# Performance work log

Hardware: AMD Instinct MI355X
Metric: run time of the kernel (lower is better)

The kernel has to match this reference:

```python
import jax, jax.numpy as jnp
import numpy as np

N = 50000        # nodes
E_RAND = 800000  # random edges (plus N self-loops)
NFEAT = 128
NHID = 64
NCLASS = 64
NHEADS = 8
ALPHA = 0.2      # leaky_relu negative slope


def setup_inputs() -> dict:
    key = jax.random.key(0)
    ks = jax.random.split(key, 7)
    x = jax.random.normal(ks[0], (N, NFEAT), jnp.float32)
    src = jax.random.randint(ks[1], (E_RAND,), 0, N, dtype=jnp.int32)
    dst = jax.random.randint(ks[2], (E_RAND,), 0, N, dtype=jnp.int32)
    loops = jnp.arange(N, dtype=jnp.int32)  # self-loops so every row has mass
    edge_index = jnp.stack([jnp.concatenate([src, loops]),
                            jnp.concatenate([dst, loops])], axis=0)  # [2, E]
    W1 = jax.random.normal(ks[3], (NHEADS, NFEAT, NHID), jnp.float32) / np.sqrt(NFEAT).astype(np.float32)
    a1 = jax.random.normal(ks[4], (NHEADS, 2 * NHID), jnp.float32) * 0.1
    W2 = jax.random.normal(ks[5], (NHEADS, NHID * NHEADS, NCLASS // NHEADS), jnp.float32) / np.sqrt(NHID * NHEADS).astype(np.float32)
    a2 = jax.random.normal(ks[6], (NHEADS, 2 * (NCLASS // NHEADS)), jnp.float32) * 0.1
    return {"x": x, "edge_index": edge_index, "W1": W1, "a1": a1, "W2": W2, "a2": a2}


def _sp_gat_head(x, src, dst, W, a):
    # SpGraphAttentionLayer (concat=True), eval mode (no dropout).
    h = x @ W                          # [N, F]
    F = h.shape[1]
    # a . [h_src || h_dst] decomposed into per-node terms (avoids [E, 2F] concat)
    s_src = h @ a[:F]                  # [N]
    s_dst = h @ a[F:]                  # [N]
    z = s_src[src] + s_dst[dst]        # [E] edge scores
    e = jnp.exp(-jax.nn.leaky_relu(z, ALPHA))  # [E] unnormalized attention
    n = h.shape[0]
    rowsum = jax.ops.segment_sum(e, src, num_segments=n)                      # [N]
    num = jax.ops.segment_sum(e[:, None] * h[dst], src, num_segments=n)       # [N, F]
    return jax.nn.elu(num / rowsum[:, None])


def reference(x, edge_index, W1, a1, W2, a2):
    src, dst = edge_index[0], edge_index[1]
    # layer 1: heads concat along feature dim -> [N, NHID*NHEADS]
    h1 = jnp.concatenate([_sp_gat_head(x, src, dst, W1[i], a1[i]) for i in range(NHEADS)], axis=1)
    # layer 2: heads concat -> [N, NCLASS]
    h2 = jnp.concatenate([_sp_gat_head(h1, src, dst, W2[i], a2[i]) for i in range(NHEADS)], axis=1)
    return h2
```

## Files before the change

kernel.cpp:

```cpp
#include <hip/hip_runtime.h>
#include <math.h>

typedef unsigned int u32;
typedef unsigned short u16;
typedef __attribute__((ext_vector_type(8))) short bf16x8;
typedef __attribute__((ext_vector_type(4))) float f32x4;
typedef __attribute__((ext_vector_type(2))) float f32x2;

static constexpr int TNFEAT  = 128;
static constexpr int TNHEADS = 8;
static constexpr int C1      = 512;
static constexpr int C2      = 64;

__device__ inline float bf2f(u16 u) {
  union { u32 i; float f; } c; c.i = ((u32)u) << 16; return c.f;
}
__device__ inline float bitsf(u32 u) {
  union { u32 i; float f; } c; c.i = u; return c.f;
}
__device__ inline u16 f2bf(float f) {
  union { float f; u32 i; } c; c.f = f;
  u32 r = c.i + 0x7FFF + ((c.i >> 16) & 1);
  return (u16)(r >> 16);
}
__device__ inline u32 cvt_pk_bf16(float lo, float hi) {
  u32 r;
  asm volatile("v_cvt_pk_bf16_f32 %0, %1, %2" : "=v"(r) : "v"(lo), "v"(hi));
  return r;
}
__device__ inline uint4 ld16(const u16* base, u32 byteoff) {
  return *reinterpret_cast<const uint4*>(reinterpret_cast<const char*>(base) + byteoff);
}
__device__ inline f32x2 up2(u32 q) {
  f32x2 p;
  p.x = bitsf(q << 16);
  p.y = bitsf(q & 0xffff0000u);
  return p;
}
__device__ inline float elu_fast(float v) {
  return v > 0.f ? v : (__expf(v) - 1.f);
}
__device__ inline int rdl_i(int v, int l) { return __builtin_amdgcn_readlane(v, l); }
__device__ inline float rdl_f(float v, int l) {
  union { float f; int i; } c; c.f = v;
  union { int i; float f; } d; d.i = __builtin_amdgcn_readlane(c.i, l);
  return d.f;
}

__global__ void k_zero(int* __restrict__ p, int n) {
  int i = blockIdx.x * blockDim.x + threadIdx.x;
  if (i < n) p[i] = 0;
}

__global__ void k_hist(const int* __restrict__ src, int* __restrict__ deg, int E) {
  int i = blockIdx.x * blockDim.x + threadIdx.x;
  if (i < E) atomicAdd(&deg[src[i]], 1);
}

__global__ __launch_bounds__(1024) void k_bscan1(const int* __restrict__ deg,
                                                 int* __restrict__ loc,
                                                 int* __restrict__ bsum, int n) {
  __shared__ int sdata[1024];
  int t = threadIdx.x;
  int i = blockIdx.x * 1024 + t;
  int v = (i < n) ? deg[i] : 0;
  sdata[t] = v;
  __syncthreads();
  for (int ofs = 1; ofs < 1024; ofs <<= 1) {
    int tv = (t >= ofs) ? sdata[t - ofs] : 0;
    __syncthreads();
    sdata[t] += tv;
    __syncthreads();
  }
  if (i < n) loc[i] = sdata[t];
  if (t == 1023) bsum[blockIdx.x] = sdata[1023];
}

__global__ void k_bscan2(int* __restrict__ bsum, int nb) {
  int t = threadIdx.x;
  int v = (t < nb) ? bsum[t] : 0;
  #pragma unroll
  for (int ofs = 1; ofs < 64; ofs <<= 1) {
    int u = __shfl_up(v, ofs);
    if (t >= ofs) v += u;
  }
  if (t < nb) bsum[t] = v;
}

__global__ __launch_bounds__(1024) void k_offs(const int* __restrict__ loc,
                                               const int* __restrict__ bsum,
                                               const int* __restrict__ deg,
                                               int* __restrict__ offs,
                                               int* __restrict__ cur, int n) {
  int b = blockIdx.x;
  int i = b * 1024 + threadIdx.x;
  int base = (b > 0) ? bsum[b - 1] : 0;
  if (i < n) {
    int v = base + loc[i];
    offs[i + 1] = v;
    cur[i] = v - deg[i];
  }
  if (i == 0) offs[0] = 0;
}

__global__ void k_fill(const int* __restrict__ src, const int* __restrict__ dst,
                       int* __restrict__ cur, int* __restrict__ adj, int E) {
  int i = blockIdx.x * blockDim.x + threadIdx.x;
  if (i < E) {
    int p = atomicAdd(&cur[src[i]], 1);
    adj[p] = dst[i];
  }
}

__global__ void k_packAll(const float* __restrict__ W1, const float* __restrict__ W2,
                          const float* __restrict__ a1,
                          u16* __restrict__ w1hi, u16* __restrict__ w1lo,
                          u16* __restrict__ w2hi, u16* __restrict__ w2lo,
                          u16* __restrict__ vhi, u16* __restrict__ vlo) {
  int b = blockIdx.x;
  if (b < 256) {
    int idx = b * 256 + threadIdx.x;
    int j = idx & 7, lane = (idx >> 3) & 63, ks = (idx >> 9) & 3, cg = idx >> 11;
    int col = cg * 16 + (lane & 15);
    int k = ks * 32 + (lane >> 4) * 8 + j;
    float f = W1[((size_t)(col >> 6) * 128 + k) * 64 + (col & 63)];
    u16 h = f2bf(f);
    w1hi[idx] = h;
    w1lo[idx] = f2bf(f - bf2f(h));
  } else if (b < 384) {
    int idx = (b - 256) * 256 + threadIdx.x;
    int j = idx & 7, lane = (idx >> 3) & 63, ks = (idx >> 9) & 15, cg = idx >> 13;
    int col = cg * 16 + (lane & 15);
    int k = ks * 32 + (lane >> 4) * 8 + j;
    float f = W2[((size_t)(col >> 3) * 512 + k) * 8 + (col & 7)];
    u16 h = f2bf(f);
    w2hi[idx] = h;
    w2lo[idx] = f2bf(f - bf2f(h));
  } else {
    int idx = (b - 384) * 256 + threadIdx.x;
    int j = idx & 7, lane = (idx >> 3) & 63, ks = idx >> 9;
    int k = ks * 32 + (lane >> 4) * 8 + j;
    int c = lane & 15;
    int h = c >> 1, s = c & 1;
    const float* wrow = W1 + ((size_t)h * 128 + k) * 64;
    const float* av = a1 + h * 128 + s * 64;
    float dot = 0.f;
    #pragma unroll 8
    for (int f = 0; f < 64; f++) dot = fmaf(wrow[f], av[f], dot);
    u16 hb = f2bf(dot);
    vhi[idx] = hb;
    vlo[idx] = f2bf(dot - bf2f(hb));
  }
}

__global__ __launch_bounds__(256) void k_xprep(const float* __restrict__ x,
        const u16* __restrict__ vhi, const u16* __restrict__ vlo,
        u16* __restrict__ xb, float* __restrict__ ss, float* __restrict__ sd, int N) {
  int w = threadIdx.x >> 6, lane = threadIdx.x & 63;
  int lr = lane & 15, lk = lane >> 4;
  int row0 = blockIdx.x * 64 + w * 16;
  f32x4 acc = {0.f, 0.f, 0.f, 0.f};
  for (int ks = 0; ks < 4; ++ks) {
    int row = row0 + lr;
    int rc = row < N ? row : 0;
    const float* ap = x + (size_t)rc * 128 + ks * 32 + lk * 8;
    float4 f0 = *reinterpret_cast<const float4*>(ap);
    float4 f1 = *reinterpret_cast<const float4*>(ap + 4);
    float fa[8] = {f0.x, f0.y, f0.z, f0.w, f1.x, f1.y, f1.z, f1.w};
    union { u32 u[4]; bf16x8 v; uint4 q; } ch, cl;
    #pragma unroll
    for (int p = 0; p < 4; ++p) {
      float e0 = fa[2 * p], e1 = fa[2 * p + 1];
      u32 h = cvt_pk_bf16(e0, e1);
      ch.u[p] = h;
      cl.u[p] = cvt_pk_bf16(e0 - bitsf(h << 16), e1 - bitsf(h & 0xffff0000u));
    }
    if (row < N)
      *reinterpret_cast<uint4*>(&xb[(size_t)row * 128 + ks * 32 + lk * 8]) = ch.q;
    size_t bidx = ((size_t)ks * 64 + lane) * 8;
    bf16x8 Bh = *reinterpret_cast<const bf16x8*>(&vhi[bidx]);
    bf16x8 Bl = *reinterpret_cast<const bf16x8*>(&vlo[bidx]);
    acc = __builtin_amdgcn_mfma_f32_16x16x32_bf16(ch.v, Bh, acc, 0, 0, 0);
    acc = __builtin_amdgcn_mfma_f32_16x16x32_bf16(cl.v, Bh, acc, 0, 0, 0);
    acc = __builtin_amdgcn_mfma_f32_16x16x32_bf16(ch.v, Bl, acc, 0, 0, 0);
  }
  int h = lr >> 1, s = lr & 1;
  float* dstp = (s == 0) ? ss : sd;
  #pragma unroll
  for (int r = 0; r < 4; ++r) {
    int row = row0 + lk * 4 + r;
    if (row < N) dstp[row * 8 + h] = acc[r];
  }
}

__global__ __launch_bounds__(256) void k_agg1x(const u16* __restrict__ xb,
        const float* __restrict__ ss, const float* __restrict__ sd,
        const int* __restrict__ offs, const int* __restrict__ adj,
        u16* __restrict__ g, int n) {
  int node = (blockIdx.x * 256 + threadIdx.x) >> 6;
  int lane = threadIdx.x & 63;
  if (node >= n) return;
  int head = lane >> 3, li = lane & 7;
  int beg = offs[node], end = offs[node + 1];
  float sS = ss[node * 8 + head];
  const char* xbb = reinterpret_cast<const char*>(xb);
  f32x2 acc2[8] = {};
  float rsum = 0.f;
  int e = beg;
  for (; e + 8 <= end; e += 8) {
    int dl = adj[e + li];
    float z = sS + sd[(u32)dl * 8u + head];
    float w = __expf(-(z > 0.f ? z : 0.2f * z));
    rsum += w;
    u32 qv[8];
    #pragma unroll
    for (int i = 0; i < 8; i++) {
      u32 di = (u32)rdl_i(dl, i);
      qv[i] = *reinterpret_cast<const u32*>(xbb + di * 256u + lane * 4u);
    }
    #pragma unroll
    for (int i = 0; i < 8; i++) {
      f32x2 xv = up2(qv[i]);
      #pragma unroll
      for (int h2 = 0; h2 < 8; h2++) {
        float wi = rdl_f(w, h2 * 8 + i);
        acc2[h2] += (f32x2){wi, wi} * xv;
      }
    }
  }
  if (e < end) {
    int m = end - e;
    int lic = li < m ? li : m - 1;
    int dl = adj[e + lic];
    float z = sS + sd[(u32)dl * 8u + head];
    float w = __expf(-(z > 0.f ? z : 0.2f * z));
    if (li >= m) w = 0.f;
    rsum += w;
    u32 qv[8];
    #pragma unroll
    for (int i = 0; i < 8; i++) {
      if (i < m) {
        u32 di = (u32)rdl_i(dl, i);
        qv[i] = *reinterpret_cast<const u32*>(xbb + di * 256u + lane * 4u);
      }
    }
    #pragma unroll
    for (int i = 0; i < 8; i++) {
      if (i < m) {
        f32x2 xv = up2(qv[i]);
        #pragma unroll
        for (int h2 = 0; h2 < 8; h2++) {
          float wi = rdl_f(w, h2 * 8 + i);
          acc2[h2] += (f32x2){wi, wi} * xv;
        }
      }
    }
  }
  rsum += __shfl_xor(rsum, 1);
  rsum += __shfl_xor(rsum, 2);
  rsum += __shfl_xor(rsum, 4);
  float inv = 1.f / rsum;
  u32* gu = reinterpret_cast<u32*>(g);
  #pragma unroll
  for (int h2 = 0; h2 < 8; h2++) {
    float ih = rdl_f(inv, h2 * 8);
    gu[((size_t)node * 8 + h2) * 64 + lane] = cvt_pk_bf16(acc2[h2].x * ih, acc2[h2].y * ih);
  }
}

__global__ __launch_bounds__(256) void k_gemm12(const u16* __restrict__ g,
        const u16* __restrict__ w1h, const u16* __restrict__ w1l,
        const u16* __restrict__ w2h, const u16* __restrict__ w2l,
        const float* __restrict__ a2,
        u16* __restrict__ h2p, float* __restrict__ ss2, float* __restrict__ sd2,
        int N) {
  __shared__ u16 h1t[32][516];
  int w = threadIdx.x >> 6, lane = threadIdx.x & 63;
  int lr = lane & 15, lk = lane >> 4;
  int row0 = blockIdx.x * 32;
  for (int hh = 0; hh < 2; ++hh) {
    int head = 2 * w + hh;
    f32x4 acc[2][4] = {};
    for (int ks = 0; ks < 4; ++ks) {
      bf16x8 Ah[2];
      #pragma unroll
      for (int rf = 0; rf < 2; ++rf) {
        int row = row0 + rf * 16 + lr;
        int rc = row < N ? row : 0;
        Ah[rf] = *reinterpret_cast<const bf16x8*>(
            &g[((size_t)rc * 8 + head) * 128 + ks * 32 + lk * 8]);
      }
      #pragma unroll
      for (int cf = 0; cf < 4; ++cf) {
        size_t bidx = ((size_t)((head * 4 + cf) * 4 + ks) * 64 + lane) * 8;
        bf16x8 Bh = *reinterpret_cast<const bf16x8*>(&w1h[bidx]);
        bf16x8 Bl = *reinterpret_cast<const bf16x8*>(&w1l[bidx]);
        #pragma unroll
        for (int rf = 0; rf < 2; ++rf) {
          acc[rf][cf] = __builtin_amdgcn_mfma_f32_16x16x32_bf16(Ah[rf], Bh, acc[rf][cf], 0, 0, 0);
          acc[rf][cf] = __builtin_amdgcn_mfma_f32_16x16x32_bf16(Ah[rf], Bl, acc[rf][cf], 0, 0, 0);
        }
      }
    }
    #pragma unroll
    for (int rf = 0; rf < 2; ++rf) {
      #pragma unroll
      for (int r = 0; r < 4; ++r) {
        int srow = rf * 16 + lk * 4 + r;
        #pragma unroll
        for (int cf = 0; cf < 4; ++cf) {
          float v = elu_fast(acc[rf][cf][r]);
          h1t[srow][head * 64 + cf * 16 + lr] = (u16)cvt_pk_bf16(v, v);
        }
      }
    }
  }
  __syncthreads();
  f32x4 accB[2] = {};
  for (int ks = 0; ks < 16; ++ks) {
    bf16x8 Ah[2];
    #pragma unroll
    for (int rf = 0; rf < 2; ++rf)
      Ah[rf] = *reinterpret_cast<const bf16x8*>(&h1t[rf * 16 + lr][ks * 32 + lk * 8]);
    size_t bidx = ((size_t)(w * 16 + ks) * 64 + lane) * 8;
    bf16x8 Bh = *reinterpret_cast<const bf16x8*>(&w2h[bidx]);
    bf16x8 Bl = *reinterpret_cast<const bf16x8*>(&w2l[bidx]);
    #pragma unroll
    for (int rf = 0; rf < 2; ++rf) {
      accB[rf] = __builtin_amdgcn_mfma_f32_16x16x32_bf16(Ah[rf], Bh, accB[rf], 0, 0, 0);
      accB[rf] = __builtin_amdgcn_mfma_f32_16x16x32_bf16(Ah[rf], Bl, accB[rf], 0, 0, 0);
    }
  }
  int hh2 = lr >> 3, jj = lr & 7;
  int headB = 2 * w + hh2;
  float aS = a2[headB * 16 + jj];
  float aD = a2[headB * 16 + 8 + jj];
  #pragma unroll
  for (int rf = 0; rf < 2; ++rf) {
    #pragma unroll
    for (int r = 0; r < 4; ++r) {
      int row = row0 + rf * 16 + lk * 4 + r;
      float val = accB[rf][r];
      if (row < N)
        h2p[(size_t)row * 64 + w * 16 + lr] = (u16)cvt_pk_bf16(val, val);
      float ps = val * aS, pd = val * aD;
      ps += __shfl_xor(ps, 1); ps += __shfl_xor(ps, 2); ps += __shfl_xor(ps, 4);
      pd += __shfl_xor(pd, 1); pd += __shfl_xor(pd, 2); pd += __shfl_xor(pd, 4);
      if (jj == 0 && row < N) {
        ss2[(size_t)row * 8 + headB] = ps;
        sd2[(size_t)row * 8 + headB] = pd;
      }
    }
  }
}

__global__ __launch_bounds__(256) void k_agg2(const u16* __restrict__ H,
        const float* __restrict__ ss, const float* __restrict__ sd,
        const int* __restrict__ offs, const int* __restrict__ adj,
        float* __restrict__ outp, int n) {
  int node = (blockIdx.x * 256 + threadIdx.x) >> 6;
  int lane = threadIdx.x & 63;
  if (node >= n) return;
  int li = lane >> 3, fg = lane & 7;
  int beg = offs[node], end = offs[node + 1];
  float sS = ss[node * 8 + fg];
  f32x2 acc2[4] = {};
  float rsum = 0.f;

  auto adj2 = [&](int e, int slot) -> u32 {
    int mm = end - e; if (mm > 16) mm = 16;
    int ii = slot < mm ? slot : mm - 1;
    return (u32)adj[e + ii];
  };

  u32 d0n = 0, d1n = 0;
  if (beg + 16 < end) { d0n = adj2(beg + 16, li); d1n = adj2(beg + 16, li + 8); }
  u32 d0 = adj2(beg, li), d1 = adj2(beg, li + 8);
  uint4 rv0 = ld16(H, d0 * 128u + fg * 16u);
  uint4 rv1 = ld16(H, d1 * 128u + fg * 16u);
  float sd0 = sd[d0 * 8u + fg], sd1 = sd[d1 * 8u + fg];

  for (int e = beg; e < end; e += 16) {
    u32 d0nn = 0, d1nn = 0;
    if (e + 32 < end) { d0nn = adj2(e + 32, li); d1nn = adj2(e + 32, li + 8); }
    int mc = end - e; if (mc > 16) mc = 16;
    float z0 = sS + sd0, z1 = sS + sd1;
    float w0 = __expf(-(z0 > 0.f ? z0 : 0.2f * z0));
    float w1 = __expf(-(z1 > 0.f ? z1 : 0.2f * z1));
    w0 = li < mc ? w0 : 0.f;
    w1 = (li + 8) < mc ? w1 : 0.f;
    rsum += w0 + w1;
    bool hn = (e + 16) < end;
    uint4 rv0N = {}, rv1N = {};
    float sd0N = 0.f, sd1N = 0.f;
    if (hn) {
      rv0N = ld16(H, d0n * 128u + fg * 16u);
      rv1N = ld16(H, d1n * 128u + fg * 16u);
      sd0N = sd[d0n * 8u + fg];
      sd1N = sd[d1n * 8u + fg];
    }
    f32x2 W0 = {w0, w0}, W1v = {w1, w1};
    acc2[0] += W0 * up2(rv0.x);
    acc2[1] += W0 * up2(rv0.y);
    acc2[2] += W0 * up2(rv0.z);
    acc2[3] += W0 * up2(rv0.w);
    acc2[0] += W1v * up2(rv1.x);
    acc2[1] += W1v * up2(rv1.y);
    acc2[2] += W1v * up2(rv1.z);
    acc2[3] += W1v * up2(rv1.w);
    if (hn) { rv0 = rv0N; rv1 = rv1N; sd0 = sd0N; sd1 = sd1N; }
    d0n = d0nn; d1n = d1nn;
  }
  #pragma unroll
  for (int mask = 8; mask < 64; mask <<= 1) {
    rsum += __shfl_xor(rsum, mask);
    #pragma unroll
    for (int k = 0; k < 4; k++) {
      acc2[k].x += __shfl_xor(acc2[k].x, mask);
      acc2[k].y += __shfl_xor(acc2[k].y, mask);
    }
  }
  if (li == 0) {
    float inv = 1.f / rsum;
    float o[8];
    #pragma unroll
    for (int k = 0; k < 4; k++) {
      o[2 * k]     = elu_fast(acc2[k].x * inv);
      o[2 * k + 1] = elu_fast(acc2[k].y * inv);
    }
    float4* Ov = reinterpret_cast<float4*>(outp);
    Ov[(size_t)node * 16 + fg * 2]     = make_float4(o[0], o[1], o[2], o[3]);
    Ov[(size_t)node * 16 + fg * 2 + 1] = make_float4(o[4], o[5], o[6], o[7]);
  }
}

extern "C" void kernel_launch(void* const* d_in, const int* in_sizes, int n_in,
                              void* d_out, int out_size, void* d_ws, size_t ws_size,
                              hipStream_t stream) {
  const float* x  = (const float*)d_in[0];
  const int*   ei = (const int*)d_in[1];
  const float* W1 = (const float*)d_in[2];
  const float* a1 = (const float*)d_in[3];
  const float* W2 = (const float*)d_in[4];
  const float* a2 = (const float*)d_in[5];
  float* out = (float*)d_out;

  int N = in_sizes[0] / TNFEAT;
  int E = in_sizes[1] / 2;
  const int* src = ei;
  const int* dst = ei + E;
  int NB = (N + 1023) / 1024;

  char* base = (char*)d_ws;
  size_t off = 0;
  auto take = [&](size_t bytes) { char* p = base + off; off = (off + bytes + 255) & ~(size_t)255; return p; };
  u16*   xb    = (u16*)take((size_t)N * TNFEAT * 2);
  u16*   g     = (u16*)take((size_t)N * 8 * TNFEAT * 2);
  u16*   h2p   = (u16*)take((size_t)N * C2 * 2);
  u16*   w1hi  = (u16*)take(65536 * 2);
  u16*   w1lo  = (u16*)take(65536 * 2);
  u16*   w2hi  = (u16*)take(32768 * 2);
  u16*   w2lo  = (u16*)take(32768 * 2);
  u16*   vhi   = (u16*)take(2048 * 2);
  u16*   vlo   = (u16*)take(2048 * 2);
  float* s1s   = (float*)take((size_t)N * 8 * 4);
  float* s1d   = (float*)take((size_t)N * 8 * 4);
  float* s2s   = (float*)take((size_t)N * 8 * 4);
  float* s2d   = (float*)take((size_t)N * 8 * 4);
  int*   deg   = (int*)take((size_t)N * 4);
  int*   offs  = (int*)take((size_t)(N + 1) * 4);
  int*   cur   = (int*)take((size_t)N * 4);
  int*   loc   = (int*)take((size_t)N * 4);
  int*   bsum  = (int*)take(64 * 4);
  int*   adj   = (int*)take((size_t)E * 4);

  hipLaunchKernelGGL(k_zero, dim3((N + 255) / 256), dim3(256), 0, stream, deg, N);
  hipLaunchKernelGGL(k_hist, dim3((E + 255) / 256), dim3(256), 0, stream, src, deg, E);
  hipLaunchKernelGGL(k_bscan1, dim3(NB), dim3(1024), 0, stream, deg, loc, bsum, N);
  hipLaunchKernelGGL(k_bscan2, dim3(1), dim3(64), 0, stream, bsum, NB);
  hipLaunchKernelGGL(k_offs, dim3(NB), dim3(1024), 0, stream, loc, bsum, deg, offs, cur, N);
  hipLaunchKernelGGL(k_fill, dim3((E + 255) / 256), dim3(256), 0, stream, src, dst, cur, adj, E);

  hipLaunchKernelGGL(k_packAll, dim3(392), dim3(256), 0, stream,
                     W1, W2, a1, w1hi, w1lo, w2hi, w2lo, vhi, vlo);

  hipLaunchKernelGGL(k_xprep, dim3((N + 63) / 64), dim3(256), 0, stream,
                     x, vhi, vlo, xb, s1s, s1d, N);
  hipLaunchKernelGGL(k_agg1x, dim3((N + 3) / 4), dim3(256), 0, stream,
                     xb, s1s, s1d, offs, adj, g, N);

  hipLaunchKernelGGL(k_gemm12, dim3((N + 31) / 32), dim3(256), 0, stream,
                     g, w1hi, w1lo, w2hi, w2lo, a2, h2p, s2s, s2d, N);

  hipLaunchKernelGGL(k_agg2, dim3((N + 3) / 4), dim3(256), 0, stream,
                     h2p, s2s, s2d, offs, adj, out, N);
}
```

Measured before the change: 245.8 us.

## Fuse layer-1 aggregation with both GEMMs in one kernel via LDS staging

Merges the layer-1 attention aggregation kernel and the layer-1/layer-2 GEMM kernel into one 1024-thread kernel. Each block aggregates 16 nodes (one wave per node) into LDS, then runs the W1 GEMM with ELU and the W2 GEMM plus attention-score projection from LDS. This removes the N×8×128 bf16 intermediate that was written to and re-read from global memory, along with one launch. In exchange LDS use per block rises, and only 4 of 16 waves do the final GEMM, which may cost occupancy and leave waves idle.

```diff
diff --git a/kernel.cpp b/kernel.cpp
--- a/kernel.cpp
+++ b/kernel.cpp
@@ -193,156 +193,155 @@
   }
 }
 
-__global__ __launch_bounds__(256) void k_agg1x(const u16* __restrict__ xb,
+__global__ __launch_bounds__(1024, 8) void k_l12(const u16* __restrict__ xb,
         const float* __restrict__ ss, const float* __restrict__ sd,
         const int* __restrict__ offs, const int* __restrict__ adj,
-        u16* __restrict__ g, int n) {
-  int node = (blockIdx.x * 256 + threadIdx.x) >> 6;
-  int lane = threadIdx.x & 63;
-  if (node >= n) return;
-  int head = lane >> 3, li = lane & 7;
-  int beg = offs[node], end = offs[node + 1];
-  float sS = ss[node * 8 + head];
-  const char* xbb = reinterpret_cast<const char*>(xb);
-  f32x2 acc2[8] = {};
-  float rsum = 0.f;
-  int e = beg;
-  for (; e + 8 <= end; e += 8) {
-    int dl = adj[e + li];
-    float z = sS + sd[(u32)dl * 8u + head];
-    float w = __expf(-(z > 0.f ? z : 0.2f * z));
-    rsum += w;
-    u32 qv[8];
-    #pragma unroll
-    for (int i = 0; i < 8; i++) {
-      u32 di = (u32)rdl_i(dl, i);
-      qv[i] = *reinterpret_cast<const u32*>(xbb + di * 256u + lane * 4u);
-    }
-    #pragma unroll
-    for (int i = 0; i < 8; i++) {
-      f32x2 xv = up2(qv[i]);
-      #pragma unroll
-      for (int h2 = 0; h2 < 8; h2++) {
-        float wi = rdl_f(w, h2 * 8 + i);
-        acc2[h2] += (f32x2){wi, wi} * xv;
-      }
-    }
-  }
-  if (e < end) {
-    int m = end - e;
-    int lic = li < m ? li : m - 1;
-    int dl = adj[e + lic];
-    float z = sS + sd[(u32)dl * 8u + head];
-    float w = __expf(-(z > 0.f ? z : 0.2f * z));
-    if (li >= m) w = 0.f;
-    rsum += w;
-    u32 qv[8];
-    #pragma unroll
-    for (int i = 0; i < 8; i++) {
-      if (i < m) {
-        u32 di = (u32)rdl_i(dl, i);
-        qv[i] = *reinterpret_cast<const u32*>(xbb + di * 256u + lane * 4u);
-      }
-    }
-    #pragma unroll
-    for (int i = 0; i < 8; i++) {
-      if (i < m) {
-        f32x2 xv = up2(qv[i]);
-        #pragma unroll
-        for (int h2 = 0; h2 < 8; h2++) {
-          float wi = rdl_f(w, h2 * 8 + i);
-          acc2[h2] += (f32x2){wi, wi} * xv;
-        }
-      }
-    }
-  }
-  rsum += __shfl_xor(rsum, 1);
-  rsum += __shfl_xor(rsum, 2);
-  rsum += __shfl_xor(rsum, 4);
-  float inv = 1.f / rsum;
-  u32* gu = reinterpret_cast<u32*>(g);
-  #pragma unroll
-  for (int h2 = 0; h2 < 8; h2++) {
-    float ih = rdl_f(inv, h2 * 8);
-    gu[((size_t)node * 8 + h2) * 64 + lane] = cvt_pk_bf16(acc2[h2].x * ih, acc2[h2].y * ih);
-  }
-}
-
-__global__ __launch_bounds__(256) void k_gemm12(const u16* __restrict__ g,
         const u16* __restrict__ w1h, const u16* __restrict__ w1l,
         const u16* __restrict__ w2h, const u16* __restrict__ w2l,
         const float* __restrict__ a2,
         u16* __restrict__ h2p, float* __restrict__ ss2, float* __restrict__ sd2,
         int N) {
-  __shared__ u16 h1t[32][516];
-  int w = threadIdx.x >> 6, lane = threadIdx.x & 63;
-  int lr = lane & 15, lk = lane >> 4;
-  int row0 = blockIdx.x * 32;
-  for (int hh = 0; hh < 2; ++hh) {
-    int head = 2 * w + hh;
-    f32x4 acc[2][4] = {};
+  __shared__ u32 g_lds[16 * 516];
+  __shared__ u16 h1t[16][516];
+  int wid = threadIdx.x >> 6;
+  int lane = threadIdx.x & 63;
+  int nodebase = blockIdx.x * 16;
+
+  {
+    int node = nodebase + wid;
+    int head = lane >> 3, li = lane & 7;
+    u32* gu = g_lds + wid * 516;
+    if (node < N) {
+      int beg = offs[node], end = offs[node + 1];
+      float sS = ss[node * 8 + head];
+      const char* xbb = reinterpret_cast<const char*>(xb);
+      f32x2 acc2[8] = {};
+      float rsum = 0.f;
+      int e = beg;
+      for (; e + 8 <= end; e += 8) {
+        int dl = adj[e + li];
+        float z = sS + sd[(u32)dl * 8u + head];
+        float w = __expf(-(z > 0.f ? z : 0.2f * z));
+        rsum += w;
+        u32 qv[8];
+        #pragma unroll
+        for (int i = 0; i < 8; i++) {
+          u32 di = (u32)rdl_i(dl, i);
+          qv[i] = *reinterpret_cast<const u32*>(xbb + di * 256u + lane * 4u);
+        }
+        #pragma unroll
+        for (int i = 0; i < 8; i++) {
+          f32x2 xv = up2(qv[i]);
+          #pragma unroll
+          for (int h2 = 0; h2 < 8; h2++) {
+            float wi = rdl_f(w, h2 * 8 + i);
+            acc2[h2] += (f32x2){wi, wi} * xv;
+          }
+        }
+      }
+      if (e < end) {
+        int m = end - e;
+        int lic = li < m ? li : m - 1;
+        int dl = adj[e + lic];
+        float z = sS + sd[(u32)dl * 8u + head];
+        float w = __expf(-(z > 0.f ? z : 0.2f * z));
+        if (li >= m) w = 0.f;
+        rsum += w;
+        u32 qv[8];
+        #pragma unroll
+        for (int i = 0; i < 8; i++) {
+          if (i < m) {
+            u32 di = (u32)rdl_i(dl, i);
+            qv[i] = *reinterpret_cast<const u32*>(xbb + di * 256u + lane * 4u);
+          }
+        }
+        #pragma unroll
+        for (int i = 0; i < 8; i++) {
+          if (i < m) {
+            f32x2 xv = up2(qv[i]);
+            #pragma unroll
+            for (int h2 = 0; h2 < 8; h2++) {
+              float wi = rdl_f(w, h2 * 8 + i);
+              acc2[h2] += (f32x2){wi, wi} * xv;
+            }
+          }
+        }
+      }
+      rsum += __shfl_xor(rsum, 1);
+      rsum += __shfl_xor(rsum, 2);
+      rsum += __shfl_xor(rsum, 4);
+      float inv = 1.f / rsum;
+      #pragma unroll
+      for (int h2 = 0; h2 < 8; h2++) {
+        float ih = rdl_f(inv, h2 * 8);
+        gu[h2 * 64 + lane] = cvt_pk_bf16(acc2[h2].x * ih, acc2[h2].y * ih);
+      }
+    } else {
+      #pragma unroll
+      for (int h2 = 0; h2 < 8; h2++) gu[h2 * 64 + lane] = 0;
+    }
+  }
+  __syncthreads();
+
+  {
+    int headA = wid >> 1;
+    int cf0 = (wid & 1) * 2;
+    int lr = lane & 15, lk = lane >> 4;
+    f32x4 acc[2] = {};
+    const char* gb = reinterpret_cast<const char*>(g_lds);
     for (int ks = 0; ks < 4; ++ks) {
-      bf16x8 Ah[2];
+      bf16x8 Ah = *reinterpret_cast<const bf16x8*>(
+          gb + lr * 2064 + headA * 256 + ks * 64 + lk * 16);
       #pragma unroll
-      for (int rf = 0; rf < 2; ++rf) {
-        int row = row0 + rf * 16 + lr;
-        int rc = row < N ? row : 0;
-        Ah[rf] = *reinterpret_cast<const bf16x8*>(
-            &g[((size_t)rc * 8 + head) * 128 + ks * 32 + lk * 8]);
-      }
-      #pragma unroll
-      for (int cf = 0; cf < 4; ++cf) {
-        size_t bidx = ((size_t)((head * 4 + cf) * 4 + ks) * 64 + lane) * 8;
+      for (int c = 0; c < 2; ++c) {
+        int cf = cf0 + c;
+        size_t bidx = ((size_t)((headA * 4 + cf) * 4 + ks) * 64 + lane) * 8;
         bf16x8 Bh = *reinterpret_cast<const bf16x8*>(&w1h[bidx]);
         bf16x8 Bl = *reinterpret_cast<const bf16x8*>(&w1l[bidx]);
-        #pragma unroll
-        for (int rf = 0; rf < 2; ++rf) {
-          acc[rf][cf] = __builtin_amdgcn_mfma_f32_16x16x32_bf16(Ah[rf], Bh, acc[rf][cf], 0, 0, 0);
-          acc[rf][cf] = __builtin_amdgcn_mfma_f32_16x16x32_bf16(Ah[rf], Bl, acc[rf][cf], 0, 0, 0);
-        }
-      }
-    }
-    #pragma unroll
-    for (int rf = 0; rf < 2; ++rf) {
-      #pragma unroll
-      for (int r = 0; r < 4; ++r) {
-        int srow = rf * 16 + lk * 4 + r;
-        #pragma unroll
-        for (int cf = 0; cf < 4; ++cf) {
-          float v = elu_fast(acc[rf][cf][r]);
-          h1t[srow][head * 64 + cf * 16 + lr] = (u16)cvt_pk_bf16(v, v);
-        }
-      }
-    }
-  }
-  __syncthreads();
-  f32x4 accB[2] = {};
-  for (int ks = 0; ks < 16; ++ks) {
-    bf16x8 Ah[2];
-    #pragma unroll
-    for (int rf = 0; rf < 2; ++rf)
-      Ah[rf] = *reinterpret_cast<const bf16x8*>(&h1t[rf * 16 + lr][ks * 32 + lk * 8]);
-    size_t bidx = ((size_t)(w * 16 + ks) * 64 + lane) * 8;
-    bf16x8 Bh = *reinterpret_cast<const bf16x8*>(&w2h[bidx]);
-    bf16x8 Bl = *reinterpret_cast<const bf16x8*>(&w2l[bidx]);
-    #pragma unroll
-    for (int rf = 0; rf < 2; ++rf) {
-      accB[rf] = __builtin_amdgcn_mfma_f32_16x16x32_bf16(Ah[rf], Bh, accB[rf], 0, 0, 0);
-      accB[rf] = __builtin_amdgcn_mfma_f32_16x16x32_bf16(Ah[rf], Bl, accB[rf], 0, 0, 0);
-    }
-  }
-  int hh2 = lr >> 3, jj = lr & 7;
-  int headB = 2 * w + hh2;
-  float aS = a2[headB * 16 + jj];
-  float aD = a2[headB * 16 + 8 + jj];
-  #pragma unroll
-  for (int rf = 0; rf < 2; ++rf) {
+        acc[c] = __builtin_amdgcn_mfma_f32_16x16x32_bf16(Ah, Bh, acc[c], 0, 0, 0);
+        acc[c] = __builtin_amdgcn_mfma_f32_16x16x32_bf16(Ah, Bl, acc[c], 0, 0, 0);
+      }
+    }
     #pragma unroll
     for (int r = 0; r < 4; ++r) {
-      int row = row0 + rf * 16 + lk * 4 + r;
-      float val = accB[rf][r];
+      int srow = lk * 4 + r;
+      #pragma unroll
+      for (int c = 0; c < 2; ++c) {
+        float v = elu_fast(acc[c][r]);
+        h1t[srow][headA * 64 + (cf0 + c) * 16 + lr] = (u16)cvt_pk_bf16(v, v);
+      }
+    }
+  }
+  __syncthreads();
+
+  if (wid < 4) {
+    int lr = lane & 15, lk = lane >> 4;
+    f32x4 acc0 = {}, acc1 = {};
+    for (int ks = 0; ks < 16; ks += 2) {
+      bf16x8 A0 = *reinterpret_cast<const bf16x8*>(&h1t[lr][ks * 32 + lk * 8]);
+      bf16x8 A1 = *reinterpret_cast<const bf16x8*>(&h1t[lr][(ks + 1) * 32 + lk * 8]);
+      size_t b0 = ((size_t)(wid * 16 + ks) * 64 + lane) * 8;
+      size_t b1 = ((size_t)(wid * 16 + ks + 1) * 64 + lane) * 8;
+      bf16x8 Bh0 = *reinterpret_cast<const bf16x8*>(&w2h[b0]);
+      bf16x8 Bl0 = *reinterpret_cast<const bf16x8*>(&w2l[b0]);
+      bf16x8 Bh1 = *reinterpret_cast<const bf16x8*>(&w2h[b1]);
+      bf16x8 Bl1 = *reinterpret_cast<const bf16x8*>(&w2l[b1]);
+      acc0 = __builtin_amdgcn_mfma_f32_16x16x32_bf16(A0, Bh0, acc0, 0, 0, 0);
+      acc1 = __builtin_amdgcn_mfma_f32_16x16x32_bf16(A1, Bh1, acc1, 0, 0, 0);
+      acc0 = __builtin_amdgcn_mfma_f32_16x16x32_bf16(A0, Bl0, acc0, 0, 0, 0);
+      acc1 = __builtin_amdgcn_mfma_f32_16x16x32_bf16(A1, Bl1, acc1, 0, 0, 0);
+    }
+    f32x4 accB = acc0 + acc1;
+    int hh2 = lr >> 3, jj = lr & 7;
+    int headB = 2 * wid + hh2;
+    float aS = a2[headB * 16 + jj];
+    float aD = a2[headB * 16 + 8 + jj];
+    #pragma unroll
+    for (int r = 0; r < 4; ++r) {
+      int row = nodebase + lk * 4 + r;
+      float val = accB[r];
       if (row < N)
-        h2p[(size_t)row * 64 + w * 16 + lr] = (u16)cvt_pk_bf16(val, val);
+        h2p[(size_t)row * 64 + wid * 16 + lr] = (u16)cvt_pk_bf16(val, val);
       float ps = val * aS, pd = val * aD;
       ps += __shfl_xor(ps, 1); ps += __shfl_xor(ps, 2); ps += __shfl_xor(ps, 4);
       pd += __shfl_xor(pd, 1); pd += __shfl_xor(pd, 2); pd += __shfl_xor(pd, 4);
@@ -455,7 +454,6 @@
   size_t off = 0;
   auto take = [&](size_t bytes) { char* p = base + off; off = (off + bytes + 255) & ~(size_t)255; return p; };
   u16*   xb    = (u16*)take((size_t)N * TNFEAT * 2);
-  u16*   g     = (u16*)take((size_t)N * 8 * TNFEAT * 2);
   u16*   h2p   = (u16*)take((size_t)N * C2 * 2);
   u16*   w1hi  = (u16*)take(65536 * 2);
   u16*   w1lo  = (u16*)take(65536 * 2);
@@ -486,11 +484,10 @@
 
   hipLaunchKernelGGL(k_xprep, dim3((N + 63) / 64), dim3(256), 0, stream,
                      x, vhi, vlo, xb, s1s, s1d, N);
-  hipLaunchKernelGGL(k_agg1x, dim3((N + 3) / 4), dim3(256), 0, stream,
-                     xb, s1s, s1d, offs, adj, g, N);
-
-  hipLaunchKernelGGL(k_gemm12, dim3((N + 31) / 32), dim3(256), 0, stream,
-                     g, w1hi, w1lo, w2hi, w2lo, a2, h2p, s2s, s2d, N);
+
+  hipLaunchKernelGGL(k_l12, dim3((N + 15) / 16), dim3(1024), 0, stream,
+                     xb, s1s, s1d, offs, adj, w1hi, w1lo, w2hi, w2lo, a2,
+                     h2p, s2s, s2d, N);
 
   hipLaunchKernelGGL(k_agg2, dim3((N + 3) / 4), dim3(256), 0, stream,
                      h2p, s2s, s2d, offs, adj, out, N);
```

Result: faster. 229.8 us (median of 2 runs) (-6.5%).
